# Optimization experiments

Hardware: AMD Instinct MI355X
Metric: run time of the kernel (lower is better)

The kernel has to match this reference:

```python
import jax, jax.numpy as jnp
import numpy as np

N, F_IN, HID, HEADS, NC, E, NG = 50000, 128, 64, 4, 8, 800000, 512


def setup_inputs() -> dict:
    key = jax.random.key(0)
    ks = jax.random.split(key, 16)
    x = jax.random.normal(ks[0], (N, F_IN), dtype=jnp.float32)
    # edges with src != dst so every node's incoming set is exactly {neighbors, self-loop}
    dst = jax.random.randint(ks[1], (E,), 0, N, dtype=jnp.int64)
    off = jax.random.randint(ks[2], (E,), 1, N, dtype=jnp.int64)
    src = (dst + off) % N
    edge_index = jnp.stack([src, dst])
    batch = jnp.sort(jax.random.randint(ks[3], (N,), 0, NG, dtype=jnp.int64))
    g = 1.0 / np.sqrt(F_IN)
    W1 = jax.random.uniform(ks[4], (F_IN, HEADS * HID), jnp.float32, -g, g)
    att_src1 = jax.random.normal(ks[5], (HEADS, HID), jnp.float32) * 0.1
    att_dst1 = jax.random.normal(ks[6], (HEADS, HID), jnp.float32) * 0.1
    b1 = jnp.zeros((HEADS * HID,), jnp.float32)
    g2 = 1.0 / np.sqrt(HEADS * HID)
    W2 = jax.random.uniform(ks[7], (HEADS * HID, HID), jnp.float32, -g2, g2)
    att_src2 = jax.random.normal(ks[8], (1, HID), jnp.float32) * 0.1
    att_dst2 = jax.random.normal(ks[9], (1, HID), jnp.float32) * 0.1
    b2 = jnp.zeros((HID,), jnp.float32)
    g3 = 1.0 / np.sqrt(HID)
    lin_w = jax.random.uniform(ks[10], (HID, NC), jnp.float32, -g3, g3)
    lin_b = jnp.zeros((NC,), jnp.float32)
    return dict(x=x, edge_index=edge_index, batch=batch, W1=W1, att_src1=att_src1,
                att_dst1=att_dst1, b1=b1, W2=W2, att_src2=att_src2, att_dst2=att_dst2,
                b2=b2, lin_w=lin_w, lin_b=lin_b)


def gat_layer(x, src, dst, W, att_s, att_d, bias, heads, out_ch):
    # PyG GATConv: h = x @ W, e_ij = LeakyReLU(a_s.h_j + a_d.h_i), softmax over dst groups
    h = (x @ W).reshape(-1, heads, out_ch)                    # [N,H,C]
    a_s = jnp.einsum('nhc,hc->nh', h, att_s)                  # [N,H]
    a_d = jnp.einsum('nhc,hc->nh', h, att_d)
    e = jax.nn.leaky_relu(a_s[src] + a_d[dst], 0.2)           # [Ef,H]
    m = jax.ops.segment_max(e, dst, num_segments=N)           # stable segment softmax
    ex = jnp.exp(e - m[dst])
    s = jax.ops.segment_sum(ex, dst, num_segments=N)
    alpha = ex / (s[dst] + 1e-16)                             # [Ef,H]
    msg = h[src] * alpha[:, :, None]                          # [Ef,H,C]
    out = jax.ops.segment_sum(msg, dst, num_segments=N)       # [N,H,C]
    return out.reshape(-1, heads * out_ch) + bias, alpha


def reference(x, edge_index, batch, W1, att_src1, att_dst1, b1,
              W2, att_src2, att_dst2, b2, lin_w, lin_b):
    loops = jnp.arange(N, dtype=edge_index.dtype)
    src = jnp.concatenate([edge_index[0], loops])             # add self-loops (PyG default)
    dst = jnp.concatenate([edge_index[1], loops])
    h, alpha1 = gat_layer(x, src, dst, W1, att_src1, att_dst1, b1, HEADS, HID)
    h = jax.nn.relu(h)
    # conv2 on edge_index_1 (already has self-loops; PyG remove+add is a no-op here)
    h, alpha2 = gat_layer(h, src, dst, W2, att_src2, att_dst2, b2, 1, HID)
    h = jax.nn.relu(h)
    sums = jax.ops.segment_sum(h, batch, num_segments=NG)     # global_mean_pool
    cnt = jax.ops.segment_sum(jnp.ones((N,), h.dtype), batch, num_segments=NG)
    pooled = sums / jnp.maximum(cnt, 1.0)[:, None]
    # dropout is identity in eval mode
    return pooled @ lin_w + lin_b
```

## Files before the change

### kernel.cpp

```cpp
#include <hip/hip_runtime.h>

#define F_IN 128
#define HID 64
#define HEADS 4
#define NC 8

typedef __bf16 bf16_t;
typedef bf16_t bf16x8 __attribute__((ext_vector_type(8)));
typedef float f32x4 __attribute__((ext_vector_type(4)));

union BF8 { bf16x8 v; ushort u[8]; };


__device__ __forceinline__ ushort f2bf(float f) {
    uint u = __float_as_uint(f);
    return (ushort)((u + 0x7fffu + ((u >> 16) & 1u)) >> 16);
}
__device__ __forceinline__ float bf2f(ushort h) {
    return __uint_as_float(((uint)h) << 16);
}
__device__ __forceinline__ float edgew(float e) {
    e = (e > 0.f) ? e : 0.2f * e;
    return __expf(e);
}

__global__ void k_setup(const float* __restrict__ W1, const float* __restrict__ W2,
                        ushort* __restrict__ w1hi,
                        ushort* __restrict__ w2hi, ushort* __restrict__ w2lo,
                        int* __restrict__ deg, int N, int* __restrict__ counts, int NG) {
    int i = blockIdx.x * blockDim.x + threadIdx.x;
    if (i < N) deg[i] = 1;
    if (i < NG) counts[i] = 0;
    if (i < 128 * 256) {
        int k = i >> 8, n = i & 255;
        int cy = n >> 7, ct = (n >> 4) & 7, c = n & 15, kc = k >> 5, ls = (k >> 3) & 3, j = k & 7;
        size_t off = ((((size_t)cy * 8 + ct) * 4 + kc) * 64 + (ls * 16 + c)) * 8 + j;
        w1hi[off] = f2bf(W1[i]);
    }
    if (i < 256 * 64) {
        int k = i >> 6, n = i & 63;
        int ct = n >> 4, c = n & 15, kc = k >> 5, ls = (k >> 3) & 3, j = k & 7;
        size_t off = (((size_t)ct * 8 + kc) * 64 + (ls * 16 + c)) * 8 + j;
        float w = W2[i];
        ushort hi = f2bf(w);
        w2hi[off] = hi; w2lo[off] = f2bf(w - bf2f(hi));
    }
}

__global__ void k_count(const int* __restrict__ ei, int E, int* __restrict__ deg,
                        const int* __restrict__ batch, int N, int* __restrict__ counts) {
    int i = blockIdx.x * blockDim.x + threadIdx.x;
    if (i < E) atomicAdd(&deg[ei[E + i]], 1);
    if (i < N) atomicAdd(&counts[batch[i]], 1);
}

__global__ __launch_bounds__(1024) void k_scan_part(const int* __restrict__ v,
                                                    int* __restrict__ excl,
                                                    int* __restrict__ bsum, int n) {
    __shared__ int buf[1024];
    int tid = threadIdx.x;
    int i = blockIdx.x * 1024 + tid;
    int val = (i < n) ? v[i] : 0;
    buf[tid] = val;
    __syncthreads();
    for (int off = 1; off < 1024; off <<= 1) {
        int t = (tid >= off) ? buf[tid - off] : 0;
        __syncthreads();
        buf[tid] += t;
        __syncthreads();
    }
    if (i < n) excl[i] = buf[tid] - val;
    if (tid == 1023) bsum[blockIdx.x] = buf[1023];
}

__global__ __launch_bounds__(1024) void k_scan_small2(const int* __restrict__ bsum,
                                                      int* __restrict__ boff, int nb,
                                                      int* __restrict__ total_out,
                                                      const int* __restrict__ counts,
                                                      int* __restrict__ gstart, int ng) {
    __shared__ int buf[1024];
    int tid = threadIdx.x;
    const int* src = (blockIdx.x == 0) ? bsum : counts;
    int cnt = (blockIdx.x == 0) ? nb : ng;
    int val = (tid < cnt) ? src[tid] : 0;
    buf[tid] = val;
    __syncthreads();
    for (int off = 1; off < 1024; off <<= 1) {
        int t = (tid >= off) ? buf[tid - off] : 0;
        __syncthreads();
        buf[tid] += t;
        __syncthreads();
    }
    if (blockIdx.x == 0) {
        if (tid < cnt) boff[tid] = buf[tid] - val;
        if (tid == 1023) total_out[0] = buf[1023];
    } else {
        if (tid < cnt) gstart[tid] = buf[tid] - val;
        if (tid == 1023) gstart[ng] = buf[1023];
    }
}

__global__ void k_scan_add_self(int* __restrict__ rowstart, const int* __restrict__ boff,
                                int* __restrict__ cursor, int* __restrict__ csr, int n) {
    int i = blockIdx.x * blockDim.x + threadIdx.x;
    if (i < n) {
        int rs = rowstart[i] + boff[i >> 10];
        rowstart[i] = rs;
        csr[rs] = i;
        cursor[i] = 1;
    }
}

__global__ void k_scatter(const int* __restrict__ ei, int E, const int* __restrict__ rowstart,
                          int* __restrict__ cursor, int* __restrict__ csr) {
    int e = blockIdx.x * blockDim.x + threadIdx.x;
    if (e < E) {
        int d = ei[E + e], s = ei[e];
        int pos = atomicAdd(&cursor[d], 1);
        csr[rowstart[d] + pos] = s;
    }
}

__global__ __launch_bounds__(256) void k_gemm1(const float* __restrict__ x,
                                               const ushort* __restrict__ w1hi,
                                               const float* __restrict__ atts,
                                               const float* __restrict__ attd,
                                               ushort* __restrict__ h1b,
                                               float* __restrict__ as1, float* __restrict__ ad1,
                                               int N) {
    __shared__ __align__(16) ushort lhi[16384];
    int tid = threadIdx.x;
    int cy = blockIdx.y;
    {
        float4* dh = (float4*)lhi; const float4* sh = (const float4*)(w1hi + (size_t)cy * 16384);
        #pragma unroll
        for (int i = 0; i < 8; i++) dh[tid + i * 256] = sh[tid + i * 256];
    }
    __syncthreads();
    int w = tid >> 6, l = tid & 63;
    int lc = l & 15, lk = l >> 4;
    int rbase = blockIdx.x * 256 + w * 64;

    f32x4 acc[4][8];
    #pragma unroll
    for (int mt = 0; mt < 4; mt++)
        #pragma unroll
        for (int ct = 0; ct < 8; ct++) acc[mt][ct] = (f32x4){0.f, 0.f, 0.f, 0.f};

    #pragma unroll
    for (int kc = 0; kc < 4; kc++) {
        BF8 ahi[4];
        #pragma unroll
        for (int mt = 0; mt < 4; mt++) {
            int row = rbase + mt * 16 + lc;
            float4 v0 = {0.f, 0.f, 0.f, 0.f}, v1 = v0;
            if (row < N) {
                const float* xp = x + (size_t)row * F_IN + kc * 32 + lk * 8;
                v0 = *(const float4*)xp; v1 = *(const float4*)(xp + 4);
            }
            float vals[8] = {v0.x, v0.y, v0.z, v0.w, v1.x, v1.y, v1.z, v1.w};
            #pragma unroll
            for (int j = 0; j < 8; j++) ahi[mt].u[j] = f2bf(vals[j]);
        }
        #pragma unroll
        for (int ct = 0; ct < 8; ct++) {
            int boff = ((ct * 4 + kc) * 64 + l) * 8;
            bf16x8 bhi = *(const bf16x8*)(lhi + boff);
            #pragma unroll
            for (int mt = 0; mt < 4; mt++) {
                acc[mt][ct] = __builtin_amdgcn_mfma_f32_16x16x32_bf16(ahi[mt].v, bhi, acc[mt][ct], 0, 0, 0);
            }
        }
    }
    #pragma unroll
    for (int mt = 0; mt < 4; mt++) {
        int rowb = rbase + mt * 16 + lk * 4;
        #pragma unroll
        for (int ct = 0; ct < 8; ct++) {
            int col = cy * 128 + ct * 16 + lc;
            #pragma unroll
            for (int r = 0; r < 4; r++) {
                int row = rowb + r;
                if (row < N) h1b[(size_t)row * 256 + col] = f2bf(acc[mt][ct][r]);
            }
        }
        #pragma unroll
        for (int hh = 0; hh < 2; hh++) {
            float s[4] = {0.f, 0.f, 0.f, 0.f}, d[4] = {0.f, 0.f, 0.f, 0.f};
            #pragma unroll
            for (int cq = 0; cq < 4; cq++) {
                int ct = hh * 4 + cq;
                int col = cy * 128 + ct * 16 + lc;
                float av = atts[col], dv = attd[col];
                #pragma unroll
                for (int r = 0; r < 4; r++) { s[r] += acc[mt][ct][r] * av; d[r] += acc[mt][ct][r] * dv; }
            }
            #pragma unroll
            for (int r = 0; r < 4; r++) {
                #pragma unroll
                for (int off = 1; off < 16; off <<= 1) {
                    s[r] += __shfl_xor(s[r], off);
                    d[r] += __shfl_xor(d[r], off);
                }
            }
            if (lc == 0) {
                int head = cy * 2 + hh;
                #pragma unroll
                for (int r = 0; r < 4; r++) {
                    int row = rowb + r;
                    if (row < N) { as1[row * 4 + head] = s[r]; ad1[row * 4 + head] = d[r]; }
                }
            }
        }
    }
}

__global__ __launch_bounds__(256) void k_gemm2(const ushort* __restrict__ xin,
                                               const ushort* __restrict__ w2hi,
                                               const ushort* __restrict__ w2lo,
                                               const float* __restrict__ atts,
                                               const float* __restrict__ attd,
                                               ushort* __restrict__ h2b,
                                               float* __restrict__ as2, float* __restrict__ ad2,
                                               int N) {
    __shared__ __align__(16) ushort lhi[16384];
    __shared__ __align__(16) ushort llo[16384];
    int tid = threadIdx.x;
    {
        float4* dh = (float4*)lhi; const float4* sh = (const float4*)w2hi;
        float4* dl = (float4*)llo; const float4* sl = (const float4*)w2lo;
        #pragma unroll
        for (int i = 0; i < 8; i++) {
            dh[tid + i * 256] = sh[tid + i * 256];
            dl[tid + i * 256] = sl[tid + i * 256];
        }
    }
    __syncthreads();
    int w = tid >> 6, l = tid & 63;
    int lc = l & 15, lk = l >> 4;
    int rbase = blockIdx.x * 256 + w * 64;

    f32x4 acc[4][4];
    #pragma unroll
    for (int mt = 0; mt < 4; mt++)
        #pragma unroll
        for (int ct = 0; ct < 4; ct++) acc[mt][ct] = (f32x4){0.f, 0.f, 0.f, 0.f};

    #pragma unroll
    for (int kc = 0; kc < 8; kc++) {
        BF8 a[4];
        #pragma unroll
        for (int mt = 0; mt < 4; mt++) {
            int row = rbase + mt * 16 + lc;
            if (row < N) {
                a[mt].v = *(const bf16x8*)(xin + (size_t)row * 256 + kc * 32 + lk * 8);
            } else {
                #pragma unroll
                for (int j = 0; j < 8; j++) a[mt].u[j] = 0;
            }
        }
        #pragma unroll
        for (int ct = 0; ct < 4; ct++) {
            int boff = ((ct * 8 + kc) * 64 + l) * 8;
            bf16x8 bhi = *(const bf16x8*)(lhi + boff);
            bf16x8 blo = *(const bf16x8*)(llo + boff);
            #pragma unroll
            for (int mt = 0; mt < 4; mt++) {
                acc[mt][ct] = __builtin_amdgcn_mfma_f32_16x16x32_bf16(a[mt].v, bhi, acc[mt][ct], 0, 0, 0);
                acc[mt][ct] = __builtin_amdgcn_mfma_f32_16x16x32_bf16(a[mt].v, blo, acc[mt][ct], 0, 0, 0);
            }
        }
    }
    #pragma unroll
    for (int mt = 0; mt < 4; mt++) {
        int rowb = rbase + mt * 16 + lk * 4;
        #pragma unroll
        for (int ct = 0; ct < 4; ct++) {
            int col = ct * 16 + lc;
            #pragma unroll
            for (int r = 0; r < 4; r++) {
                int row = rowb + r;
                if (row < N) h2b[(size_t)row * 64 + col] = f2bf(acc[mt][ct][r]);
            }
        }
        float s[4] = {0.f, 0.f, 0.f, 0.f}, d[4] = {0.f, 0.f, 0.f, 0.f};
        #pragma unroll
        for (int ct = 0; ct < 4; ct++) {
            int col = ct * 16 + lc;
            float av = atts[col], dv = attd[col];
            #pragma unroll
            for (int r = 0; r < 4; r++) { s[r] += acc[mt][ct][r] * av; d[r] += acc[mt][ct][r] * dv; }
        }
        #pragma unroll
        for (int r = 0; r < 4; r++) {
            #pragma unroll
            for (int off = 1; off < 16; off <<= 1) {
                s[r] += __shfl_xor(s[r], off);
                d[r] += __shfl_xor(d[r], off);
            }
        }
        if (lc == 0) {
            #pragma unroll
            for (int r = 0; r < 4; r++) {
                int row = rowb + r;
                if (row < N) { as2[row] = s[r]; ad2[row] = d[r]; }
            }
        }
    }
}

__global__ __launch_bounds__(256) void k_fagg1(const ushort* __restrict__ h1b,
                                               const float* __restrict__ as1,
                                               const float* __restrict__ ad1,
                                               const int* __restrict__ rowstart,
                                               const int* __restrict__ csr,
                                               const float* __restrict__ b1,
                                               ushort* __restrict__ out1b, int N) {
    __shared__ float lw[4][256];
    __shared__ int   lsrc[4][64];
    int wid = threadIdx.x >> 6, lane = threadIdx.x & 63;
    int n = blockIdx.x * 4 + wid;
    if (n >= N) return;
    int beg = rowstart[n], end = rowstart[n + 1];
    float4 adv = *(const float4*)(ad1 + (size_t)n * 4);
    int lh = lane & 31, half = lane >> 5;
    int c0 = lh * 8;
    int head = lh >> 3;
    float s0 = 0.f, s1 = 0.f, s2 = 0.f, s3 = 0.f;
    float a[8];
    #pragma unroll
    for (int i = 0; i < 8; i++) a[i] = 0.f;

    for (int jc = beg; jc < end; jc += 64) {
        int j = jc + lane;
        float4 wv = {0.f, 0.f, 0.f, 0.f};
        int src = 0;
        if (j < end) {
            src = csr[j];
            float4 av = *(const float4*)(as1 + (size_t)src * 4);
            wv.x = edgew(av.x + adv.x); wv.y = edgew(av.y + adv.y);
            wv.z = edgew(av.z + adv.z); wv.w = edgew(av.w + adv.w);
            s0 += wv.x; s1 += wv.y; s2 += wv.z; s3 += wv.w;
        }
        *(float4*)&lw[wid][lane * 4] = wv;
        lsrc[wid][lane] = src;
        int cnt = min(64, end - jc);
        int pairs = (cnt + 1) >> 1;
        for (int t = 0; t < pairs; t += 8) {
            #pragma unroll
            for (int u = 0; u < 8; u++) {
                int tt = t + u;
                if (tt < pairs) {
                    int e = 2 * tt + half;
                    int sr = lsrc[wid][e];
                    float wgt = lw[wid][e * 4 + head];
                    uint4 hv = *(const uint4*)(h1b + (size_t)sr * 256 + c0);
                    a[0] += wgt * bf2f((ushort)(hv.x & 0xffffu));
                    a[1] += wgt * bf2f((ushort)(hv.x >> 16));
                    a[2] += wgt * bf2f((ushort)(hv.y & 0xffffu));
                    a[3] += wgt * bf2f((ushort)(hv.y >> 16));
                    a[4] += wgt * bf2f((ushort)(hv.z & 0xffffu));
                    a[5] += wgt * bf2f((ushort)(hv.z >> 16));
                    a[6] += wgt * bf2f((ushort)(hv.w & 0xffffu));
                    a[7] += wgt * bf2f((ushort)(hv.w >> 16));
                }
            }
        }
    }
    #pragma unroll
    for (int i = 0; i < 8; i++) a[i] += __shfl_xor(a[i], 32);
    #pragma unroll
    for (int off = 1; off < 64; off <<= 1) {
        s0 += __shfl_xor(s0, off); s1 += __shfl_xor(s1, off);
        s2 += __shfl_xor(s2, off); s3 += __shfl_xor(s3, off);
    }
    float sv = (head == 0) ? s0 : (head == 1) ? s1 : (head == 2) ? s2 : s3;
    float inv = 1.f / sv;
    if (half == 0) {
        const float4* bv = (const float4*)(b1 + c0);
        float4 bA = bv[0], bB = bv[1];
        float o0 = fmaxf(a[0] * inv + bA.x, 0.f), o1 = fmaxf(a[1] * inv + bA.y, 0.f);
        float o2 = fmaxf(a[2] * inv + bA.z, 0.f), o3 = fmaxf(a[3] * inv + bA.w, 0.f);
        float o4 = fmaxf(a[4] * inv + bB.x, 0.f), o5 = fmaxf(a[5] * inv + bB.y, 0.f);
        float o6 = fmaxf(a[6] * inv + bB.z, 0.f), o7 = fmaxf(a[7] * inv + bB.w, 0.f);
        uint4 ov;
        ov.x = (uint)f2bf(o0) | ((uint)f2bf(o1) << 16);
        ov.y = (uint)f2bf(o2) | ((uint)f2bf(o3) << 16);
        ov.z = (uint)f2bf(o4) | ((uint)f2bf(o5) << 16);
        ov.w = (uint)f2bf(o6) | ((uint)f2bf(o7) << 16);
        *(uint4*)(out1b + (size_t)n * 256 + c0) = ov;
    }
}

__global__ __launch_bounds__(256) void k_fagg2(const ushort* __restrict__ h2b,
                                               const float* __restrict__ as2,
                                               const float* __restrict__ ad2,
                                               const int* __restrict__ rowstart,
                                               const int* __restrict__ csr,
                                               const float* __restrict__ b2,
                                               float* __restrict__ out2, int N) {
    __shared__ float lw[4][64];
    __shared__ int   lsrc[4][64];
    int wid = threadIdx.x >> 6, lane = threadIdx.x & 63;
    int n = blockIdx.x * 4 + wid;
    if (n >= N) return;
    int beg = rowstart[n], end = rowstart[n + 1];
    float adv = ad2[n];
    int g = lane >> 3, li = lane & 7;
    int c0 = li * 8;
    float ss = 0.f;
    float a[8];
    #pragma unroll
    for (int i = 0; i < 8; i++) a[i] = 0.f;

    for (int jc = beg; jc < end; jc += 64) {
        int j = jc + lane;
        float wgt = 0.f;
        int src = 0;
        if (j < end) {
            src = csr[j];
            wgt = edgew(as2[src] + adv);
            ss += wgt;
        }
        lw[wid][lane] = wgt;
        lsrc[wid][lane] = src;
        int cnt = min(64, end - jc);
        int groups = (cnt + 7) >> 3;
        for (int t = 0; t < groups; t += 2) {
            #pragma unroll
            for (int u = 0; u < 2; u++) {
                int tt = t + u;
                if (tt < groups) {
                    int e = tt * 8 + g;
                    int sr = lsrc[wid][e];
                    float wv = lw[wid][e];
                    uint4 hv = *(const uint4*)(h2b + (size_t)sr * 64 + c0);
                    a[0] += wv * bf2f((ushort)(hv.x & 0xffffu));
                    a[1] += wv * bf2f((ushort)(hv.x >> 16));
                    a[2] += wv * bf2f((ushort)(hv.y & 0xffffu));
                    a[3] += wv * bf2f((ushort)(hv.y >> 16));
                    a[4] += wv * bf2f((ushort)(hv.z & 0xffffu));
                    a[5] += wv * bf2f((ushort)(hv.z >> 16));
                    a[6] += wv * bf2f((ushort)(hv.w & 0xffffu));
                    a[7] += wv * bf2f((ushort)(hv.w >> 16));
                }
            }
        }
    }
    #pragma unroll
    for (int i = 0; i < 8; i++) {
        a[i] += __shfl_xor(a[i], 8);
        a[i] += __shfl_xor(a[i], 16);
        a[i] += __shfl_xor(a[i], 32);
    }
    #pragma unroll
    for (int off = 1; off < 64; off <<= 1) ss += __shfl_xor(ss, off);
    float inv = 1.f / ss;
    if (g == 0) {
        const float4* bv = (const float4*)(b2 + c0);
        float4 bA = bv[0], bB = bv[1];
        float4 oA, oB;
        oA.x = fmaxf(a[0] * inv + bA.x, 0.f); oA.y = fmaxf(a[1] * inv + bA.y, 0.f);
        oA.z = fmaxf(a[2] * inv + bA.z, 0.f); oA.w = fmaxf(a[3] * inv + bA.w, 0.f);
        oB.x = fmaxf(a[4] * inv + bB.x, 0.f); oB.y = fmaxf(a[5] * inv + bB.y, 0.f);
        oB.z = fmaxf(a[6] * inv + bB.z, 0.f); oB.w = fmaxf(a[7] * inv + bB.w, 0.f);
        float* op = out2 + (size_t)n * 64 + c0;
        *(float4*)op = oA;
        *(float4*)(op + 4) = oB;
    }
}


__global__ __launch_bounds__(64) void k_pool(const float* __restrict__ out2,
                                             const int* __restrict__ gstart,
                                             const float* __restrict__ lin_w,
                                             const float* __restrict__ lin_b,
                                             float* __restrict__ out, int NG) {
    __shared__ float mean[64];
    int g = blockIdx.x;
    int lane = threadIdx.x;
    int beg = gstart[g], end = gstart[g + 1];
    float s = 0.f;
    for (int n = beg; n < end; n++) s += out2[(size_t)n * 64 + lane];
    float cnt = (float)(end - beg);
    mean[lane] = s / fmaxf(cnt, 1.f);
    __syncthreads();
    if (lane < NC) {
        float acc = lin_b[lane];
        #pragma unroll
        for (int c = 0; c < 64; c++) acc += mean[c] * lin_w[c * NC + lane];
        out[g * NC + lane] = acc;
    }
}


extern "C" void kernel_launch(void* const* d_in, const int* in_sizes, int n_in,
                              void* d_out, int out_size, void* d_ws, size_t ws_size,
                              hipStream_t stream) {
    const float* x      = (const float*)d_in[0];
    const int*   ei     = (const int*)d_in[1];
    const int*   batch  = (const int*)d_in[2];
    const float* W1     = (const float*)d_in[3];
    const float* att_s1 = (const float*)d_in[4];
    const float* att_d1 = (const float*)d_in[5];
    const float* b1     = (const float*)d_in[6];
    const float* W2     = (const float*)d_in[7];
    const float* att_s2 = (const float*)d_in[8];
    const float* att_d2 = (const float*)d_in[9];
    const float* b2     = (const float*)d_in[10];
    const float* lin_w  = (const float*)d_in[11];
    const float* lin_b  = (const float*)d_in[12];
    float* out = (float*)d_out;

    const int N  = in_sizes[0] / F_IN;
    const int E  = in_sizes[1] / 2;
    const int NG = out_size / NC;
    const int NE = E + N;
    const int NB = (N + 1023) / 1024;

    char* p = (char*)d_ws;
    auto alloc = [&](size_t bytes) { char* r = p; p += (bytes + 255) & ~(size_t)255; return r; };
    ushort* h1b     = (ushort*)alloc(sizeof(ushort) * (size_t)N * 256);
    ushort* out1b   = (ushort*)alloc(sizeof(ushort) * (size_t)N * 256);
    ushort* h2b     = (ushort*)alloc(sizeof(ushort) * (size_t)N * 64);
    float*  out2    = (float*)alloc(sizeof(float) * (size_t)N * 64);
    float*  as1     = (float*)alloc(sizeof(float) * (size_t)N * 4);
    float*  ad1     = (float*)alloc(sizeof(float) * (size_t)N * 4);
    float*  as2     = (float*)alloc(sizeof(float) * (size_t)N);
    float*  ad2     = (float*)alloc(sizeof(float) * (size_t)N);
    int*    rowstart= (int*)alloc(sizeof(int) * (size_t)(N + 1));
    int*    itmp    = (int*)alloc(sizeof(int) * (size_t)N);
    int*    csr     = (int*)alloc(sizeof(int) * (size_t)NE);
    int*    counts  = (int*)alloc(sizeof(int) * (size_t)NG);
    int*    gstart  = (int*)alloc(sizeof(int) * (size_t)(NG + 1));
    int*    bsum    = (int*)alloc(sizeof(int) * 1024);
    int*    boff    = (int*)alloc(sizeof(int) * 1024);
    ushort* w1hi    = (ushort*)alloc(sizeof(ushort) * 32768);
    ushort* w2hi    = (ushort*)alloc(sizeof(ushort) * 16384);
    ushort* w2lo    = (ushort*)alloc(sizeof(ushort) * 16384);

    int bs = 256;
    k_setup<<<(N + bs - 1) / bs, bs, 0, stream>>>(W1, W2, w1hi, w2hi, w2lo,
                                                  itmp, N, counts, NG);
    k_count<<<(E + bs - 1) / bs, bs, 0, stream>>>(ei, E, itmp, batch, N, counts);
    k_scan_part<<<NB, 1024, 0, stream>>>(itmp, rowstart, bsum, N);
    k_scan_small2<<<2, 1024, 0, stream>>>(bsum, boff, NB, rowstart + N, counts, gstart, NG);
    k_scan_add_self<<<(N + 1023) / 1024, 1024, 0, stream>>>(rowstart, boff, itmp, csr, N);
    k_scatter<<<(E + bs - 1) / bs, bs, 0, stream>>>(ei, E, rowstart, itmp, csr);

    k_gemm1<<<dim3((N + 255) / 256, 2), 256, 0, stream>>>(x, w1hi, att_s1, att_d1, h1b, as1, ad1, N);
    k_fagg1<<<(N + 3) / 4, 256, 0, stream>>>(h1b, as1, ad1, rowstart, csr, b1, out1b, N);

    k_gemm2<<<(N + 255) / 256, 256, 0, stream>>>(out1b, w2hi, w2lo, att_s2, att_d2, h2b, as2, ad2, N);
    k_fagg2<<<(N + 3) / 4, 256, 0, stream>>>(h2b, as2, ad2, rowstart, csr, b2, out2, N);

    k_pool<<<NG, 64, 0, stream>>>(out2, gstart, lin_w, lin_b, out, NG);
}
```

Before: 303.2 us.

## Reorder layer-1 GAT to aggregate raw features before the weight GEMM

Layer 1 now folds the attention vectors into W1 (W1·att), so the attention logits come straight from x in a light projection kernel. Aggregation then gathers 128-wide bf16 x rows per edge instead of 256-wide h1 rows, writing one aggregated 128-vector per head. A per-head GEMM with bias and ReLU follows. This halves the gather traffic per edge, but it adds a 4x-wide intermediate (N×512 bf16), more FMAs per edge (four heads times eight channels per lane), and an extra kernel launch.

Result: slower. 317.5 us (+4.7%).

```diff
diff --git a/kernel.cpp b/kernel.cpp
--- a/kernel.cpp
+++ b/kernel.cpp
@@ -25,17 +25,20 @@
 }
 
 __global__ void k_setup(const float* __restrict__ W1, const float* __restrict__ W2,
-                        ushort* __restrict__ w1hi,
+                        const float* __restrict__ atts1, const float* __restrict__ attd1,
+                        ushort* __restrict__ w1p,
                         ushort* __restrict__ w2hi, ushort* __restrict__ w2lo,
+                        float* __restrict__ ps, float* __restrict__ pd,
                         int* __restrict__ deg, int N, int* __restrict__ counts, int NG) {
     int i = blockIdx.x * blockDim.x + threadIdx.x;
     if (i < N) deg[i] = 1;
     if (i < NG) counts[i] = 0;
     if (i < 128 * 256) {
         int k = i >> 8, n = i & 255;
-        int cy = n >> 7, ct = (n >> 4) & 7, c = n & 15, kc = k >> 5, ls = (k >> 3) & 3, j = k & 7;
-        size_t off = ((((size_t)cy * 8 + ct) * 4 + kc) * 64 + (ls * 16 + c)) * 8 + j;
-        w1hi[off] = f2bf(W1[i]);
+        int h = n >> 6, c = n & 63;
+        int ct = c >> 4, lc = c & 15, kc = k >> 5, ls = (k >> 3) & 3, j = k & 7;
+        size_t off = ((((size_t)h * 4 + ct) * 4 + kc) * 64 + (ls * 16 + lc)) * 8 + j;
+        w1p[off] = f2bf(W1[i]);
     }
     if (i < 256 * 64) {
         int k = i >> 6, n = i & 63;
@@ -44,6 +47,16 @@
         float w = W2[i];
         ushort hi = f2bf(w);
         w2hi[off] = hi; w2lo[off] = f2bf(w - bf2f(hi));
+    }
+    if (i < 512) {
+        int h = i >> 7, k = i & 127;
+        float s = 0.f, d = 0.f;
+        for (int c = 0; c < 64; c++) {
+            float w = W1[k * 256 + h * 64 + c];
+            s += w * atts1[h * 64 + c];
+            d += w * attd1[h * 64 + c];
+        }
+        ps[i] = s; pd[i] = d;
     }
 }
 
@@ -121,54 +134,177 @@
     }
 }
 
-__global__ __launch_bounds__(256) void k_gemm1(const float* __restrict__ x,
-                                               const ushort* __restrict__ w1hi,
-                                               const float* __restrict__ atts,
-                                               const float* __restrict__ attd,
-                                               ushort* __restrict__ h1b,
-                                               float* __restrict__ as1, float* __restrict__ ad1,
-                                               int N) {
-    __shared__ __align__(16) ushort lhi[16384];
+__global__ __launch_bounds__(256) void k_proj(const float* __restrict__ x,
+                                              const float* __restrict__ ps,
+                                              const float* __restrict__ pd,
+                                              ushort* __restrict__ xb,
+                                              float* __restrict__ as1, float* __restrict__ ad1,
+                                              int N) {
+    __shared__ float lps[512], lpd[512];
     int tid = threadIdx.x;
-    int cy = blockIdx.y;
+    lps[tid] = ps[tid]; lps[tid + 256] = ps[tid + 256];
+    lpd[tid] = pd[tid]; lpd[tid + 256] = pd[tid + 256];
+    __syncthreads();
+    int wid = tid >> 6, lane = tid & 63;
+    int n = blockIdx.x * 4 + wid;
+    if (n >= N) return;
+    float2 xv = *(const float2*)(x + (size_t)n * 128 + lane * 2);
+    ushort2 xbv; xbv.x = f2bf(xv.x); xbv.y = f2bf(xv.y);
+    *(ushort2*)(xb + (size_t)n * 128 + lane * 2) = xbv;
+    float s[4], d[4];
+    #pragma unroll
+    for (int h = 0; h < 4; h++) {
+        s[h] = xv.x * lps[h * 128 + 2 * lane] + xv.y * lps[h * 128 + 2 * lane + 1];
+        d[h] = xv.x * lpd[h * 128 + 2 * lane] + xv.y * lpd[h * 128 + 2 * lane + 1];
+    }
+    #pragma unroll
+    for (int off = 1; off < 64; off <<= 1) {
+        #pragma unroll
+        for (int h = 0; h < 4; h++) {
+            s[h] += __shfl_xor(s[h], off);
+            d[h] += __shfl_xor(d[h], off);
+        }
+    }
+    if (lane == 0) {
+        float4 sv = {s[0], s[1], s[2], s[3]};
+        float4 dv = {d[0], d[1], d[2], d[3]};
+        *(float4*)(as1 + (size_t)n * 4) = sv;
+        *(float4*)(ad1 + (size_t)n * 4) = dv;
+    }
+}
+
+__global__ __launch_bounds__(256) void k_fagg1(const ushort* __restrict__ xb,
+                                               const float* __restrict__ as1,
+                                               const float* __restrict__ ad1,
+                                               const int* __restrict__ rowstart,
+                                               const int* __restrict__ csr,
+                                               ushort* __restrict__ xaggb, int N) {
+    __shared__ float lw[4][256];
+    __shared__ int   lsrc[4][64];
+    int wid = threadIdx.x >> 6, lane = threadIdx.x & 63;
+    int n = blockIdx.x * 4 + wid;
+    if (n >= N) return;
+    int beg = rowstart[n], end = rowstart[n + 1];
+    float4 adv = *(const float4*)(ad1 + (size_t)n * 4);
+    int g = lane >> 4, li = lane & 15;
+    int c0 = li * 8;
+    float s0 = 0.f, s1 = 0.f, s2 = 0.f, s3 = 0.f;
+    float a[4][8];
+    #pragma unroll
+    for (int h = 0; h < 4; h++)
+        #pragma unroll
+        for (int c = 0; c < 8; c++) a[h][c] = 0.f;
+
+    for (int jc = beg; jc < end; jc += 64) {
+        int j = jc + lane;
+        float4 wv = {0.f, 0.f, 0.f, 0.f};
+        int src = 0;
+        if (j < end) {
+            src = csr[j];
+            float4 av = *(const float4*)(as1 + (size_t)src * 4);
+            wv.x = edgew(av.x + adv.x); wv.y = edgew(av.y + adv.y);
+            wv.z = edgew(av.z + adv.z); wv.w = edgew(av.w + adv.w);
+            s0 += wv.x; s1 += wv.y; s2 += wv.z; s3 += wv.w;
+        }
+        *(float4*)&lw[wid][lane * 4] = wv;
+        lsrc[wid][lane] = src;
+        int cnt = min(64, end - jc);
+        int iters = (cnt + 3) >> 2;
+        for (int t = 0; t < iters; t += 4) {
+            #pragma unroll
+            for (int u = 0; u < 4; u++) {
+                int tt = t + u;
+                if (tt < iters) {
+                    int e = tt * 4 + g;
+                    int sr = lsrc[wid][e];
+                    float w0 = lw[wid][e * 4 + 0], w1 = lw[wid][e * 4 + 1];
+                    float w2 = lw[wid][e * 4 + 2], w3 = lw[wid][e * 4 + 3];
+                    uint4 hv = *(const uint4*)(xb + (size_t)sr * 128 + c0);
+                    float v[8];
+                    v[0] = bf2f((ushort)(hv.x & 0xffffu)); v[1] = bf2f((ushort)(hv.x >> 16));
+                    v[2] = bf2f((ushort)(hv.y & 0xffffu)); v[3] = bf2f((ushort)(hv.y >> 16));
+                    v[4] = bf2f((ushort)(hv.z & 0xffffu)); v[5] = bf2f((ushort)(hv.z >> 16));
+                    v[6] = bf2f((ushort)(hv.w & 0xffffu)); v[7] = bf2f((ushort)(hv.w >> 16));
+                    #pragma unroll
+                    for (int c = 0; c < 8; c++) {
+                        a[0][c] += w0 * v[c];
+                        a[1][c] += w1 * v[c];
+                        a[2][c] += w2 * v[c];
+                        a[3][c] += w3 * v[c];
+                    }
+                }
+            }
+        }
+    }
+    #pragma unroll
+    for (int h = 0; h < 4; h++)
+        #pragma unroll
+        for (int c = 0; c < 8; c++) {
+            a[h][c] += __shfl_xor(a[h][c], 16);
+            a[h][c] += __shfl_xor(a[h][c], 32);
+        }
+    #pragma unroll
+    for (int off = 1; off < 64; off <<= 1) {
+        s0 += __shfl_xor(s0, off); s1 += __shfl_xor(s1, off);
+        s2 += __shfl_xor(s2, off); s3 += __shfl_xor(s3, off);
+    }
+    if (g == 0) {
+        float inv[4] = {1.f / s0, 1.f / s1, 1.f / s2, 1.f / s3};
+        #pragma unroll
+        for (int h = 0; h < 4; h++) {
+            uint4 ov;
+            ov.x = (uint)f2bf(a[h][0] * inv[h]) | ((uint)f2bf(a[h][1] * inv[h]) << 16);
+            ov.y = (uint)f2bf(a[h][2] * inv[h]) | ((uint)f2bf(a[h][3] * inv[h]) << 16);
+            ov.z = (uint)f2bf(a[h][4] * inv[h]) | ((uint)f2bf(a[h][5] * inv[h]) << 16);
+            ov.w = (uint)f2bf(a[h][6] * inv[h]) | ((uint)f2bf(a[h][7] * inv[h]) << 16);
+            *(uint4*)(xaggb + ((size_t)h * N + n) * 128 + c0) = ov;
+        }
+    }
+}
+
+__global__ __launch_bounds__(256) void k_postgemm(const ushort* __restrict__ xaggb,
+                                                  const ushort* __restrict__ w1p,
+                                                  const float* __restrict__ b1,
+                                                  ushort* __restrict__ out1b, int N) {
+    __shared__ __align__(16) ushort lw[8192];
+    int tid = threadIdx.x;
+    int h = blockIdx.y;
     {
-        float4* dh = (float4*)lhi; const float4* sh = (const float4*)(w1hi + (size_t)cy * 16384);
-        #pragma unroll
-        for (int i = 0; i < 8; i++) dh[tid + i * 256] = sh[tid + i * 256];
+        float4* dh = (float4*)lw; const float4* sh = (const float4*)(w1p + (size_t)h * 8192);
+        #pragma unroll
+        for (int i = 0; i < 4; i++) dh[tid + i * 256] = sh[tid + i * 256];
     }
     __syncthreads();
     int w = tid >> 6, l = tid & 63;
     int lc = l & 15, lk = l >> 4;
     int rbase = blockIdx.x * 256 + w * 64;
-
-    f32x4 acc[4][8];
+    const ushort* abase = xaggb + (size_t)h * N * 128;
+
+    f32x4 acc[4][4];
     #pragma unroll
     for (int mt = 0; mt < 4; mt++)
         #pragma unroll
-        for (int ct = 0; ct < 8; ct++) acc[mt][ct] = (f32x4){0.f, 0.f, 0.f, 0.f};
+        for (int ct = 0; ct < 4; ct++) acc[mt][ct] = (f32x4){0.f, 0.f, 0.f, 0.f};
 
     #pragma unroll
     for (int kc = 0; kc < 4; kc++) {
-        BF8 ahi[4];
+        BF8 a[4];
         #pragma unroll
         for (int mt = 0; mt < 4; mt++) {
             int row = rbase + mt * 16 + lc;
-            float4 v0 = {0.f, 0.f, 0.f, 0.f}, v1 = v0;
             if (row < N) {
-                const float* xp = x + (size_t)row * F_IN + kc * 32 + lk * 8;
-                v0 = *(const float4*)xp; v1 = *(const float4*)(xp + 4);
-            }
-            float vals[8] = {v0.x, v0.y, v0.z, v0.w, v1.x, v1.y, v1.z, v1.w};
-            #pragma unroll
-            for (int j = 0; j < 8; j++) ahi[mt].u[j] = f2bf(vals[j]);
-        }
-        #pragma unroll
-        for (int ct = 0; ct < 8; ct++) {
-            int boff = ((ct * 4 + kc) * 64 + l) * 8;
-            bf16x8 bhi = *(const bf16x8*)(lhi + boff);
+                a[mt].v = *(const bf16x8*)(abase + (size_t)row * 128 + kc * 32 + lk * 8);
+            } else {
+                #pragma unroll
+                for (int j = 0; j < 8; j++) a[mt].u[j] = 0;
+            }
+        }
+        #pragma unroll
+        for (int ct = 0; ct < 4; ct++) {
+            bf16x8 bv = *(const bf16x8*)(lw + ((ct * 4 + kc) * 64 + l) * 8);
             #pragma unroll
             for (int mt = 0; mt < 4; mt++) {
-                acc[mt][ct] = __builtin_amdgcn_mfma_f32_16x16x32_bf16(ahi[mt].v, bhi, acc[mt][ct], 0, 0, 0);
+                acc[mt][ct] = __builtin_amdgcn_mfma_f32_16x16x32_bf16(a[mt].v, bv, acc[mt][ct], 0, 0, 0);
             }
         }
     }
@@ -176,39 +312,15 @@
     for (int mt = 0; mt < 4; mt++) {
         int rowb = rbase + mt * 16 + lk * 4;
         #pragma unroll
-        for (int ct = 0; ct < 8; ct++) {
-            int col = cy * 128 + ct * 16 + lc;
+        for (int ct = 0; ct < 4; ct++) {
+            int col = h * 64 + ct * 16 + lc;
+            float bb = b1[col];
             #pragma unroll
             for (int r = 0; r < 4; r++) {
                 int row = rowb + r;
-                if (row < N) h1b[(size_t)row * 256 + col] = f2bf(acc[mt][ct][r]);
-            }
-        }
-        #pragma unroll
-        for (int hh = 0; hh < 2; hh++) {
-            float s[4] = {0.f, 0.f, 0.f, 0.f}, d[4] = {0.f, 0.f, 0.f, 0.f};
-            #pragma unroll
-            for (int cq = 0; cq < 4; cq++) {
-                int ct = hh * 4 + cq;
-                int col = cy * 128 + ct * 16 + lc;
-                float av = atts[col], dv = attd[col];
-                #pragma unroll
-                for (int r = 0; r < 4; r++) { s[r] += acc[mt][ct][r] * av; d[r] += acc[mt][ct][r] * dv; }
-            }
-            #pragma unroll
-            for (int r = 0; r < 4; r++) {
-                #pragma unroll
-                for (int off = 1; off < 16; off <<= 1) {
-                    s[r] += __shfl_xor(s[r], off);
-                    d[r] += __shfl_xor(d[r], off);
-                }
-            }
-            if (lc == 0) {
-                int head = cy * 2 + hh;
-                #pragma unroll
-                for (int r = 0; r < 4; r++) {
-                    int row = rowb + r;
-                    if (row < N) { as1[row * 4 + head] = s[r]; ad1[row * 4 + head] = d[r]; }
+                if (row < N) {
+                    float o = acc[mt][ct][r] + bb;
+                    out1b[(size_t)row * 256 + col] = f2bf(o > 0.f ? o : 0.f);
                 }
             }
         }
@@ -306,89 +418,6 @@
                 if (row < N) { as2[row] = s[r]; ad2[row] = d[r]; }
             }
         }
-    }
-}
-
-__global__ __launch_bounds__(256) void k_fagg1(const ushort* __restrict__ h1b,
-                                               const float* __restrict__ as1,
-                                               const float* __restrict__ ad1,
-                                               const int* __restrict__ rowstart,
-                                               const int* __restrict__ csr,
-                                               const float* __restrict__ b1,
-                                               ushort* __restrict__ out1b, int N) {
-    __shared__ float lw[4][256];
-    __shared__ int   lsrc[4][64];
-    int wid = threadIdx.x >> 6, lane = threadIdx.x & 63;
-    int n = blockIdx.x * 4 + wid;
-    if (n >= N) return;
-    int beg = rowstart[n], end = rowstart[n + 1];
-    float4 adv = *(const float4*)(ad1 + (size_t)n * 4);
-    int lh = lane & 31, half = lane >> 5;
-    int c0 = lh * 8;
-    int head = lh >> 3;
-    float s0 = 0.f, s1 = 0.f, s2 = 0.f, s3 = 0.f;
-    float a[8];
-    #pragma unroll
-    for (int i = 0; i < 8; i++) a[i] = 0.f;
-
-    for (int jc = beg; jc < end; jc += 64) {
-        int j = jc + lane;
-        float4 wv = {0.f, 0.f, 0.f, 0.f};
-        int src = 0;
-        if (j < end) {
-            src = csr[j];
-            float4 av = *(const float4*)(as1 + (size_t)src * 4);
-            wv.x = edgew(av.x + adv.x); wv.y = edgew(av.y + adv.y);
-            wv.z = edgew(av.z + adv.z); wv.w = edgew(av.w + adv.w);
-            s0 += wv.x; s1 += wv.y; s2 += wv.z; s3 += wv.w;
-        }
-        *(float4*)&lw[wid][lane * 4] = wv;
-        lsrc[wid][lane] = src;
-        int cnt = min(64, end - jc);
-        int pairs = (cnt + 1) >> 1;
-        for (int t = 0; t < pairs; t += 8) {
-            #pragma unroll
-            for (int u = 0; u < 8; u++) {
-                int tt = t + u;
-                if (tt < pairs) {
-                    int e = 2 * tt + half;
-                    int sr = lsrc[wid][e];
-                    float wgt = lw[wid][e * 4 + head];
-                    uint4 hv = *(const uint4*)(h1b + (size_t)sr * 256 + c0);
-                    a[0] += wgt * bf2f((ushort)(hv.x & 0xffffu));
-                    a[1] += wgt * bf2f((ushort)(hv.x >> 16));
-                    a[2] += wgt * bf2f((ushort)(hv.y & 0xffffu));
-                    a[3] += wgt * bf2f((ushort)(hv.y >> 16));
-                    a[4] += wgt * bf2f((ushort)(hv.z & 0xffffu));
-                    a[5] += wgt * bf2f((ushort)(hv.z >> 16));
-                    a[6] += wgt * bf2f((ushort)(hv.w & 0xffffu));
-                    a[7] += wgt * bf2f((ushort)(hv.w >> 16));
-                }
-            }
-        }
-    }
-    #pragma unroll
-    for (int i = 0; i < 8; i++) a[i] += __shfl_xor(a[i], 32);
-    #pragma unroll
-    for (int off = 1; off < 64; off <<= 1) {
-        s0 += __shfl_xor(s0, off); s1 += __shfl_xor(s1, off);
-        s2 += __shfl_xor(s2, off); s3 += __shfl_xor(s3, off);
-    }
-    float sv = (head == 0) ? s0 : (head == 1) ? s1 : (head == 2) ? s2 : s3;
-    float inv = 1.f / sv;
-    if (half == 0) {
-        const float4* bv = (const float4*)(b1 + c0);
-        float4 bA = bv[0], bB = bv[1];
-        float o0 = fmaxf(a[0] * inv + bA.x, 0.f), o1 = fmaxf(a[1] * inv + bA.y, 0.f);
-        float o2 = fmaxf(a[2] * inv + bA.z, 0.f), o3 = fmaxf(a[3] * inv + bA.w, 0.f);
-        float o4 = fmaxf(a[4] * inv + bB.x, 0.f), o5 = fmaxf(a[5] * inv + bB.y, 0.f);
-        float o6 = fmaxf(a[6] * inv + bB.z, 0.f), o7 = fmaxf(a[7] * inv + bB.w, 0.f);
-        uint4 ov;
-        ov.x = (uint)f2bf(o0) | ((uint)f2bf(o1) << 16);
-        ov.y = (uint)f2bf(o2) | ((uint)f2bf(o3) << 16);
-        ov.z = (uint)f2bf(o4) | ((uint)f2bf(o5) << 16);
-        ov.w = (uint)f2bf(o6) | ((uint)f2bf(o7) << 16);
-        *(uint4*)(out1b + (size_t)n * 256 + c0) = ov;
     }
 }
 
@@ -520,10 +549,10 @@
 
     char* p = (char*)d_ws;
     auto alloc = [&](size_t bytes) { char* r = p; p += (bytes + 255) & ~(size_t)255; return r; };
-    ushort* h1b     = (ushort*)alloc(sizeof(ushort) * (size_t)N * 256);
+    ushort* xb      = (ushort*)alloc(sizeof(ushort) * (size_t)N * 128);
+    ushort* xaggb   = (ushort*)alloc(sizeof(ushort) * (size_t)N * 512);
     ushort* out1b   = (ushort*)alloc(sizeof(ushort) * (size_t)N * 256);
     ushort* h2b     = (ushort*)alloc(sizeof(ushort) * (size_t)N * 64);
-    float*  out2    = (float*)alloc(sizeof(float) * (size_t)N * 64);
     float*  as1     = (float*)alloc(sizeof(float) * (size_t)N * 4);
     float*  ad1     = (float*)alloc(sizeof(float) * (size_t)N * 4);
     float*  as2     = (float*)alloc(sizeof(float) * (size_t)N);
@@ -535,21 +564,25 @@
     int*    gstart  = (int*)alloc(sizeof(int) * (size_t)(NG + 1));
     int*    bsum    = (int*)alloc(sizeof(int) * 1024);
     int*    boff    = (int*)alloc(sizeof(int) * 1024);
-    ushort* w1hi    = (ushort*)alloc(sizeof(ushort) * 32768);
+    ushort* w1p     = (ushort*)alloc(sizeof(ushort) * 32768);
     ushort* w2hi    = (ushort*)alloc(sizeof(ushort) * 16384);
     ushort* w2lo    = (ushort*)alloc(sizeof(ushort) * 16384);
+    float*  psv     = (float*)alloc(sizeof(float) * 512);
+    float*  pdv     = (float*)alloc(sizeof(float) * 512);
+    float*  out2    = (float*)xb;
 
     int bs = 256;
-    k_setup<<<(N + bs - 1) / bs, bs, 0, stream>>>(W1, W2, w1hi, w2hi, w2lo,
-                                                  itmp, N, counts, NG);
+    k_setup<<<(N + bs - 1) / bs, bs, 0, stream>>>(W1, W2, att_s1, att_d1, w1p, w2hi, w2lo,
+                                                  psv, pdv, itmp, N, counts, NG);
     k_count<<<(E + bs - 1) / bs, bs, 0, stream>>>(ei, E, itmp, batch, N, counts);
     k_scan_part<<<NB, 1024, 0, stream>>>(itmp, rowstart, bsum, N);
     k_scan_small2<<<2, 1024, 0, stream>>>(bsum, boff, NB, rowstart + N, counts, gstart, NG);
     k_scan_add_self<<<(N + 1023) / 1024, 1024, 0, stream>>>(rowstart, boff, itmp, csr, N);
     k_scatter<<<(E + bs - 1) / bs, bs, 0, stream>>>(ei, E, rowstart, itmp, csr);
 
-    k_gemm1<<<dim3((N + 255) / 256, 2), 256, 0, stream>>>(x, w1hi, att_s1, att_d1, h1b, as1, ad1, N);
-    k_fagg1<<<(N + 3) / 4, 256, 0, stream>>>(h1b, as1, ad1, rowstart, csr, b1, out1b, N);
+    k_proj<<<(N + 3) / 4, 256, 0, stream>>>(x, psv, pdv, xb, as1, ad1, N);
+    k_fagg1<<<(N + 3) / 4, 256, 0, stream>>>(xb, as1, ad1, rowstart, csr, xaggb, N);
+    k_postgemm<<<dim3((N + 255) / 256, 4), 256, 0, stream>>>(xaggb, w1p, b1, out1b, N);
 
     k_gemm2<<<(N + 255) / 256, 256, 0, stream>>>(out1b, w2hi, w2lo, att_s2, att_d2, h2b, as2, ad2, N);
     k_fagg2<<<(N + 3) / 4, 256, 0, stream>>>(h2b, as2, ad2, rowstart, csr, b2, out2, N);
```
